# Performance work log

Measured on AMD Instinct MI355X. Metric: run time of the kernel, lower is better.

Reference implementation:

```python
import jax, jax.numpy as jnp
import numpy as np

B, S, H, NH = 2, 2048, 1024, 16
HD = H // NH  # 64
EPS = 1e-5


def setup_inputs() -> dict:
    key = jax.random.key(0)
    ks = jax.random.split(key, 4)
    return {
        "hidden_states": jax.random.normal(ks[0], (B, S, H), dtype=jnp.float32),
        "W_attn": jax.random.normal(ks[1], (H, 3 * H), dtype=jnp.float32) * (1.0 / np.sqrt(H)),
        "b_attn": jnp.zeros((3 * H,), dtype=jnp.float32),
        "W_proj": jax.random.normal(ks[2], (H, H), dtype=jnp.float32) * (1.0 / np.sqrt(H)),
        "b_proj": jnp.zeros((H,), dtype=jnp.float32),
        "q_gamma": jnp.ones((HD,), dtype=jnp.float32),
        "q_beta": jnp.zeros((HD,), dtype=jnp.float32),
        "k_gamma": jnp.ones((HD,), dtype=jnp.float32),
        "k_beta": jnp.zeros((HD,), dtype=jnp.float32),
    }


def _layernorm(x, gamma, beta):
    mu = jnp.mean(x, axis=-1, keepdims=True)
    var = jnp.mean(jnp.square(x - mu), axis=-1, keepdims=True)
    return (x - mu) * jax.lax.rsqrt(var + EPS) * gamma + beta


def reference(hidden_states, W_attn, b_attn, W_proj, b_proj, q_gamma, q_beta, k_gamma, k_beta):
    b, s, h = hidden_states.shape
    qkv = hidden_states @ W_attn + b_attn  # [B,S,3H]
    q, k, v = jnp.split(qkv, 3, axis=-1)
    # [B,S,H] -> [B,NH,S,HD]
    def to_heads(t):
        return t.reshape(b, s, NH, HD).transpose(0, 2, 1, 3)
    q, k, v = to_heads(q), to_heads(k), to_heads(v)
    # QK LayerNorm over head_dim
    q = _layernorm(q, q_gamma, q_beta)
    k = _layernorm(k, k_gamma, k_beta)
    scale = HD ** (-0.5)
    scores = jnp.einsum("bhqd,bhkd->bhqk", q, k) * scale
    causal = jnp.tril(jnp.ones((s, s), dtype=bool))
    mask_value = jnp.finfo(scores.dtype).min
    scores = jnp.where(causal, scores, mask_value)
    attn = jax.nn.softmax(scores.astype(jnp.float32), axis=-1).astype(q.dtype)
    out = jnp.einsum("bhqk,bhkd->bhqd", attn, v)
    out = out.transpose(0, 2, 1, 3).reshape(b, s, h)
    out = out @ W_proj + b_proj
    return out
```

## Files before the change

kernel.cpp:

```cpp
#include <hip/hip_runtime.h>
#include <hip/hip_bf16.h>

typedef __bf16 bf16x8 __attribute__((ext_vector_type(8)));
typedef float f32x4 __attribute__((ext_vector_type(4)));

#define EPS 1e-5f
#define QSCALE 0.18033688011112042f

__device__ __forceinline__ unsigned short f2bf(float f) {
  union { float f; unsigned int i; } c; c.f = f;
  unsigned int r = c.i + 0x7FFFu + ((c.i >> 16) & 1u);
  return (unsigned short)(r >> 16);
}
__device__ __forceinline__ unsigned short f2bf_t(float f) {
  union { float f; unsigned int i; } c; c.f = f;
  return (unsigned short)(c.i >> 16);
}

__device__ __forceinline__ void glds16(const void* g, void* l) {
  __builtin_amdgcn_global_load_lds(
      (const __attribute__((address_space(1))) unsigned int*)g,
      (__attribute__((address_space(3))) unsigned int*)l, 16, 0, 0);
}

__device__ __forceinline__ void transpose_tile(
    const float* __restrict__ in, unsigned short* __restrict__ out,
    int R, int C, int ct0, int rt0, unsigned short* S )
{
  const int t = threadIdx.x;
  const int r = t >> 2, c4 = (t & 3) * 16;
  {
    long base = (long)(rt0 + r) * C + ct0 + c4;
    float4 a = *(const float4*)&in[base];
    float4 b = *(const float4*)&in[base + 4];
    float4 c = *(const float4*)&in[base + 8];
    float4 d = *(const float4*)&in[base + 12];
    unsigned short v[16] = {f2bf(a.x), f2bf(a.y), f2bf(a.z), f2bf(a.w),
                            f2bf(b.x), f2bf(b.y), f2bf(b.z), f2bf(b.w),
                            f2bf(c.x), f2bf(c.y), f2bf(c.z), f2bf(c.w),
                            f2bf(d.x), f2bf(d.y), f2bf(d.z), f2bf(d.w)};
    *(uint4*)&S[r * 72 + c4]     = *(uint4*)&v[0];
    *(uint4*)&S[r * 72 + c4 + 8] = *(uint4*)&v[8];
  }
  __syncthreads();
  unsigned short tmp[16];
#pragma unroll
  for (int j = 0; j < 16; j++) tmp[j] = S[(c4 + j) * 72 + r];
  *(uint4*)&out[(long)(ct0 + r) * R + rt0 + c4]     = *(uint4*)&tmp[0];
  *(uint4*)&out[(long)(ct0 + r) * R + rt0 + c4 + 8] = *(uint4*)&tmp[8];
}

__global__ __launch_bounds__(256) void prep_kernel(
    const float* __restrict__ Wa, const float* __restrict__ Wp,
    const float* __restrict__ X,
    unsigned short* __restrict__ WaT, unsigned short* __restrict__ WpT,
    unsigned short* __restrict__ Xbf)
{
  __shared__ __align__(16) unsigned short S[64 * 72];
  const int id = blockIdx.x;
  if (id < 768) {
    transpose_tile(Wa, WaT, 1024, 3072, (id % 48) * 64, (id / 48) * 64, S);
  } else if (id < 1024) {
    const int i2 = id - 768;
    transpose_tile(Wp, WpT, 1024, 1024, (i2 % 16) * 64, (i2 / 16) * 64, S);
  } else {
    long i = ((long)(id - 1024) * 256 + threadIdx.x) * 16;
    float4 a = *(const float4*)&X[i];
    float4 b = *(const float4*)&X[i + 4];
    float4 c = *(const float4*)&X[i + 8];
    float4 d = *(const float4*)&X[i + 12];
    unsigned short v[16] = {f2bf(a.x), f2bf(a.y), f2bf(a.z), f2bf(a.w),
                            f2bf(b.x), f2bf(b.y), f2bf(b.z), f2bf(b.w),
                            f2bf(c.x), f2bf(c.y), f2bf(c.z), f2bf(c.w),
                            f2bf(d.x), f2bf(d.y), f2bf(d.z), f2bf(d.w)};
    *(uint4*)&Xbf[i]     = *(uint4*)&v[0];
    *(uint4*)&Xbf[i + 8] = *(uint4*)&v[8];
  }
}

__global__ __launch_bounds__(256) void qkvt_kernel(
    const float* __restrict__ Xf,
    const unsigned short* __restrict__ Xbf, int use_xbf,
    const unsigned short* __restrict__ WT,
    const float* __restrict__ bias,
    const float* __restrict__ qg, const float* __restrict__ qb,
    const float* __restrict__ kg, const float* __restrict__ kb,
    unsigned short* __restrict__ Qws, unsigned short* __restrict__ Kws,
    unsigned short* __restrict__ Vt)
{
  __shared__ __align__(16) unsigned short As[3][128 * 32];
  __shared__ __align__(16) unsigned short Bs[3][128 * 32];

  const int tid = threadIdx.x;
  const int w = tid >> 6, lane = tid & 63, quad = lane >> 4, l15 = lane & 15;
  const int mh = w & 1, nh = w >> 1;
  const int id = blockIdx.x;
  const int grow = lane >> 2, gcol = (lane & 3) * 8;

  f32x4 acc[4][4];
#pragma unroll
  for (int i = 0; i < 4; i++)
#pragma unroll
    for (int j = 0; j < 4; j++) acc[i][j] = (f32x4){0.f, 0.f, 0.f, 0.f};

  if (id < 512) {
    const int n0 = (id & 15) * 128, m0 = (id >> 4) * 128;

    if (use_xbf) {
      const long ga = (long)(m0 + w * 32 + grow) * 1024 + gcol;
      const long gb = (long)(n0 + w * 32 + grow) * 1024 + gcol;
#define STAGE_QK(bf, kk) do { \
        glds16(&Xbf[ga + (kk)],             &As[bf][(w * 32) * 32]); \
        glds16(&Xbf[ga + (kk) + 16 * 1024], &As[bf][(w * 32 + 16) * 32]); \
        glds16(&WT[gb + (kk)],              &Bs[bf][(w * 32) * 32]); \
        glds16(&WT[gb + (kk) + 16 * 1024],  &Bs[bf][(w * 32 + 16) * 32]); \
      } while (0)
      STAGE_QK(0, 0);
      STAGE_QK(1, 32);
      asm volatile("s_waitcnt vmcnt(4)" ::: "memory");
      __builtin_amdgcn_s_barrier();
      __builtin_amdgcn_sched_barrier(0);

      int cur = 0;
      for (int kt = 0; kt < 1024; kt += 32) {
        int stg = cur + 2; if (stg >= 3) stg -= 3;
        if (kt + 64 < 1024) STAGE_QK(stg, kt + 64);
        bf16x8 af[4], bfr[4];
#pragma unroll
        for (int mq = 0; mq < 4; mq++)
          af[mq] = *(const bf16x8*)&As[cur][(mh * 64 + mq * 16 + l15) * 32 + quad * 8];
#pragma unroll
        for (int nq = 0; nq < 4; nq++)
          bfr[nq] = *(const bf16x8*)&Bs[cur][(nh * 64 + nq * 16 + l15) * 32 + quad * 8];
#pragma unroll
        for (int mq = 0; mq < 4; mq++)
#pragma unroll
          for (int nq = 0; nq < 4; nq++)
            acc[mq][nq] = __builtin_amdgcn_mfma_f32_16x16x32_bf16(af[mq], bfr[nq], acc[mq][nq], 0, 0, 0);
        if (kt + 32 < 1024) {
          if (kt + 64 < 1024) asm volatile("s_waitcnt vmcnt(4)" ::: "memory");
          else                asm volatile("s_waitcnt vmcnt(0)" ::: "memory");
          __builtin_amdgcn_s_barrier();
          __builtin_amdgcn_sched_barrier(0);
        }
        cur = cur + 1; if (cur >= 3) cur -= 3;
      }
#undef STAGE_QK
    } else {
      const int sr2 = tid >> 1, sh2 = (tid & 1) * 16;
      {
        long xo = (long)(m0 + sr2) * 1024 + sh2;
        float4 a0 = *(const float4*)&Xf[xo];
        float4 a1 = *(const float4*)&Xf[xo + 4];
        float4 a2 = *(const float4*)&Xf[xo + 8];
        float4 a3 = *(const float4*)&Xf[xo + 12];
        unsigned short v[16] = {f2bf(a0.x), f2bf(a0.y), f2bf(a0.z), f2bf(a0.w),
                                f2bf(a1.x), f2bf(a1.y), f2bf(a1.z), f2bf(a1.w),
                                f2bf(a2.x), f2bf(a2.y), f2bf(a2.z), f2bf(a2.w),
                                f2bf(a3.x), f2bf(a3.y), f2bf(a3.z), f2bf(a3.w)};
        *(uint4*)&As[0][sr2 * 32 + sh2]     = *(uint4*)&v[0];
        *(uint4*)&As[0][sr2 * 32 + sh2 + 8] = *(uint4*)&v[8];
        long wo = (long)(n0 + sr2) * 1024 + sh2;
        *(uint4*)&Bs[0][sr2 * 32 + sh2]     = *(const uint4*)&WT[wo];
        *(uint4*)&Bs[0][sr2 * 32 + sh2 + 8] = *(const uint4*)&WT[wo + 8];
      }
      __syncthreads();

      int buf = 0;
      for (int kt = 0; kt < 1024; kt += 32) {
        const int nbuf = buf ^ 1;
        const bool pf = (kt + 32) < 1024;
        uint4 wv0, wv1;
        float4 a0, a1, a2, a3;
        if (pf) {
          long xo = (long)(m0 + sr2) * 1024 + kt + 32 + sh2;
          a0 = *(const float4*)&Xf[xo];
          a1 = *(const float4*)&Xf[xo + 4];
          a2 = *(const float4*)&Xf[xo + 8];
          a3 = *(const float4*)&Xf[xo + 12];
          long wo = (long)(n0 + sr2) * 1024 + kt + 32 + sh2;
          wv0 = *(const uint4*)&WT[wo];
          wv1 = *(const uint4*)&WT[wo + 8];
        }

        bf16x8 af[4], bfr[4];
#pragma unroll
        for (int mq = 0; mq < 4; mq++)
          af[mq] = *(const bf16x8*)&As[buf][(mh * 64 + mq * 16 + l15) * 32 + quad * 8];
#pragma unroll
        for (int nq = 0; nq < 4; nq++)
          bfr[nq] = *(const bf16x8*)&Bs[buf][(nh * 64 + nq * 16 + l15) * 32 + quad * 8];
#pragma unroll
        for (int mq = 0; mq < 4; mq++)
#pragma unroll
          for (int nq = 0; nq < 4; nq++)
            acc[mq][nq] = __builtin_amdgcn_mfma_f32_16x16x32_bf16(af[mq], bfr[nq], acc[mq][nq], 0, 0, 0);

        if (pf) {
          unsigned short v[16] = {f2bf(a0.x), f2bf(a0.y), f2bf(a0.z), f2bf(a0.w),
                                  f2bf(a1.x), f2bf(a1.y), f2bf(a1.z), f2bf(a1.w),
                                  f2bf(a2.x), f2bf(a2.y), f2bf(a2.z), f2bf(a2.w),
                                  f2bf(a3.x), f2bf(a3.y), f2bf(a3.z), f2bf(a3.w)};
          *(uint4*)&As[nbuf][sr2 * 32 + sh2]     = *(uint4*)&v[0];
          *(uint4*)&As[nbuf][sr2 * 32 + sh2 + 8] = *(uint4*)&v[8];
          *(uint4*)&Bs[nbuf][sr2 * 32 + sh2]     = wv0;
          *(uint4*)&Bs[nbuf][sr2 * 32 + sh2 + 8] = wv1;
        }
        __syncthreads();
        buf = nbuf;
      }
    }

#pragma unroll
    for (int nq = 0; nq < 4; nq++) {
      float bv = bias[n0 + nh * 64 + nq * 16 + l15];
#pragma unroll
      for (int mq = 0; mq < 4; mq++)
#pragma unroll
        for (int rr = 0; rr < 4; rr++) acc[mq][nq][rr] += bv;
    }

    const int g = (n0 >> 6) + nh;
    const bool isQ = g < 16;
    {
      float gv[4], bev[4];
#pragma unroll
      for (int nq = 0; nq < 4; nq++) {
        int d = nq * 16 + l15;
        gv[nq]  = isQ ? qg[d] : kg[d];
        bev[nq] = isQ ? qb[d] : kb[d];
        if (isQ) { gv[nq] *= QSCALE; bev[nq] *= QSCALE; }
      }
#pragma unroll
      for (int mq = 0; mq < 4; mq++)
#pragma unroll
        for (int rr = 0; rr < 4; rr++) {
          float s  = acc[mq][0][rr] + acc[mq][1][rr] + acc[mq][2][rr] + acc[mq][3][rr];
          float s2 = acc[mq][0][rr]*acc[mq][0][rr] + acc[mq][1][rr]*acc[mq][1][rr]
                   + acc[mq][2][rr]*acc[mq][2][rr] + acc[mq][3][rr]*acc[mq][3][rr];
#pragma unroll
          for (int off = 1; off < 16; off <<= 1) {
            s  += __shfl_xor(s,  off, 64);
            s2 += __shfl_xor(s2, off, 64);
          }
          float mu   = s * (1.0f / 64.0f);
          float var  = fmaxf(s2 * (1.0f / 64.0f) - mu * mu, 0.f);
          float rstd = rsqrtf(var + EPS);
#pragma unroll
          for (int nq = 0; nq < 4; nq++)
            acc[mq][nq][rr] = (acc[mq][nq][rr] - mu) * rstd * gv[nq] + bev[nq];
        }
    }

    unsigned short* dst = isQ ? Qws : Kws;
    const int head = isQ ? g : g - 16;
#pragma unroll
    for (int mq = 0; mq < 4; mq++)
#pragma unroll
      for (int rr = 0; rr < 4; rr++) {
        int m = m0 + mh * 64 + mq * 16 + quad * 4 + rr;
        int b = m >> 11, s = m & 2047;
        long base = ((long)((b * 16 + head) * 2048 + s)) * 64;
#pragma unroll
        for (int nq = 0; nq < 4; nq++)
          dst[base + nq * 16 + l15] = f2bf(acc[mq][nq][rr]);
      }
  } else {
    const int id2 = id - 512;
    const int n0 = (id2 & 15) * 128, m0 = ((id2 >> 4) & 7) * 128, bz = id2 >> 7;
    const long xrow0 = (long)bz * 2048;
    const unsigned short* WvT = WT + 2048L * 1024;

    if (use_xbf) {
      const long gva = (long)(m0 + w * 32 + grow) * 1024 + gcol;
      const long gvb = (xrow0 + n0 + w * 32 + grow) * 1024 + gcol;
#define STAGE_V(bf, kk) do { \
        glds16(&WvT[gva + (kk)],             &As[bf][(w * 32) * 32]); \
        glds16(&WvT[gva + (kk) + 16 * 1024], &As[bf][(w * 32 + 16) * 32]); \
        glds16(&Xbf[gvb + (kk)],             &Bs[bf][(w * 32) * 32]); \
        glds16(&Xbf[gvb + (kk) + 16 * 1024], &Bs[bf][(w * 32 + 16) * 32]); \
      } while (0)
      STAGE_V(0, 0);
      STAGE_V(1, 32);
      asm volatile("s_waitcnt vmcnt(4)" ::: "memory");
      __builtin_amdgcn_s_barrier();
      __builtin_amdgcn_sched_barrier(0);

      int cur = 0;
      for (int kt = 0; kt < 1024; kt += 32) {
        int stg = cur + 2; if (stg >= 3) stg -= 3;
        if (kt + 64 < 1024) STAGE_V(stg, kt + 64);
        bf16x8 af[4], bfr[4];
#pragma unroll
        for (int mq = 0; mq < 4; mq++)
          af[mq] = *(const bf16x8*)&As[cur][(mh * 64 + mq * 16 + l15) * 32 + quad * 8];
#pragma unroll
        for (int nq = 0; nq < 4; nq++)
          bfr[nq] = *(const bf16x8*)&Bs[cur][(nh * 64 + nq * 16 + l15) * 32 + quad * 8];
#pragma unroll
        for (int mq = 0; mq < 4; mq++)
#pragma unroll
          for (int nq = 0; nq < 4; nq++)
            acc[mq][nq] = __builtin_amdgcn_mfma_f32_16x16x32_bf16(af[mq], bfr[nq], acc[mq][nq], 0, 0, 0);
        if (kt + 32 < 1024) {
          if (kt + 64 < 1024) asm volatile("s_waitcnt vmcnt(4)" ::: "memory");
          else                asm volatile("s_waitcnt vmcnt(0)" ::: "memory");
          __builtin_amdgcn_s_barrier();
          __builtin_amdgcn_sched_barrier(0);
        }
        cur = cur + 1; if (cur >= 3) cur -= 3;
      }
#undef STAGE_V
    } else {
      const int sr2 = tid >> 1, sh2 = (tid & 1) * 16;
      {
        long wo = (long)(m0 + sr2) * 1024 + sh2;
        *(uint4*)&As[0][sr2 * 32 + sh2]     = *(const uint4*)&WvT[wo];
        *(uint4*)&As[0][sr2 * 32 + sh2 + 8] = *(const uint4*)&WvT[wo + 8];
        long xo = (xrow0 + n0 + sr2) * 1024 + sh2;
        float4 a0 = *(const float4*)&Xf[xo];
        float4 a1 = *(const float4*)&Xf[xo + 4];
        float4 a2 = *(const float4*)&Xf[xo + 8];
        float4 a3 = *(const float4*)&Xf[xo + 12];
        unsigned short v[16] = {f2bf(a0.x), f2bf(a0.y), f2bf(a0.z), f2bf(a0.w),
                                f2bf(a1.x), f2bf(a1.y), f2bf(a1.z), f2bf(a1.w),
                                f2bf(a2.x), f2bf(a2.y), f2bf(a2.z), f2bf(a2.w),
                                f2bf(a3.x), f2bf(a3.y), f2bf(a3.z), f2bf(a3.w)};
        *(uint4*)&Bs[0][sr2 * 32 + sh2]     = *(uint4*)&v[0];
        *(uint4*)&Bs[0][sr2 * 32 + sh2 + 8] = *(uint4*)&v[8];
      }
      __syncthreads();

      int buf = 0;
      for (int kt = 0; kt < 1024; kt += 32) {
        const int nbuf = buf ^ 1;
        const bool pf = (kt + 32) < 1024;
        uint4 wv0, wv1;
        float4 a0, a1, a2, a3;
        if (pf) {
          long wo = (long)(m0 + sr2) * 1024 + kt + 32 + sh2;
          wv0 = *(const uint4*)&WvT[wo];
          wv1 = *(const uint4*)&WvT[wo + 8];
          long xo = (xrow0 + n0 + sr2) * 1024 + kt + 32 + sh2;
          a0 = *(const float4*)&Xf[xo];
          a1 = *(const float4*)&Xf[xo + 4];
          a2 = *(const float4*)&Xf[xo + 8];
          a3 = *(const float4*)&Xf[xo + 12];
        }

        bf16x8 af[4], bfr[4];
#pragma unroll
        for (int mq = 0; mq < 4; mq++)
          af[mq] = *(const bf16x8*)&As[buf][(mh * 64 + mq * 16 + l15) * 32 + quad * 8];
#pragma unroll
        for (int nq = 0; nq < 4; nq++)
          bfr[nq] = *(const bf16x8*)&Bs[buf][(nh * 64 + nq * 16 + l15) * 32 + quad * 8];
#pragma unroll
        for (int mq = 0; mq < 4; mq++)
#pragma unroll
          for (int nq = 0; nq < 4; nq++)
            acc[mq][nq] = __builtin_amdgcn_mfma_f32_16x16x32_bf16(af[mq], bfr[nq], acc[mq][nq], 0, 0, 0);

        if (pf) {
          *(uint4*)&As[nbuf][sr2 * 32 + sh2]     = wv0;
          *(uint4*)&As[nbuf][sr2 * 32 + sh2 + 8] = wv1;
          unsigned short v[16] = {f2bf(a0.x), f2bf(a0.y), f2bf(a0.z), f2bf(a0.w),
                                  f2bf(a1.x), f2bf(a1.y), f2bf(a1.z), f2bf(a1.w),
                                  f2bf(a2.x), f2bf(a2.y), f2bf(a2.z), f2bf(a2.w),
                                  f2bf(a3.x), f2bf(a3.y), f2bf(a3.z), f2bf(a3.w)};
          *(uint4*)&Bs[nbuf][sr2 * 32 + sh2]     = *(uint4*)&v[0];
          *(uint4*)&Bs[nbuf][sr2 * 32 + sh2 + 8] = *(uint4*)&v[8];
        }
        __syncthreads();
        buf = nbuf;
      }
    }

    const long outb = (long)bz * 2097152;
#pragma unroll
    for (int mq = 0; mq < 4; mq++)
#pragma unroll
      for (int rr = 0; rr < 4; rr++) {
        int m = m0 + mh * 64 + mq * 16 + quad * 4 + rr;
        float bv = bias[2048 + m];
#pragma unroll
        for (int nq = 0; nq < 4; nq++) {
          int n = n0 + nh * 64 + nq * 16 + l15;
          Vt[outb + (long)m * 2048 + n] = f2bf(acc[mq][nq][rr] + bv);
        }
      }
  }
}

__global__ __launch_bounds__(256) void attn_kernel(
    unsigned short* __restrict__ Qws,
    const unsigned short* __restrict__ Kws,
    const unsigned short* __restrict__ Vt)
{
  __shared__ __align__(16) unsigned short Ks[2][64 * 72];
  __shared__ __align__(16) unsigned short VTs[2][64 * 72];
  __shared__ __align__(16) unsigned short Ps[64 * 64];

  const int tid = threadIdx.x;
  const int w = tid >> 6, lane = tid & 63, quad = lane >> 4, l15 = lane & 15;
  const int id = blockIdx.x;
  const int bh = (id & 7) * 4 + ((id >> 3) & 3);
  const int x  = id >> 5;
  const long bhoff = (long)bh * 2048 * 64;
  const long bhv   = (long)bh * 131072;

  const int sr = tid >> 2, sc = (tid & 3) * 16;
  const int qsw = ((sr >> 2) & 3) << 4;
  const int sw = ((l15 >> 2) & 3) << 4;
  const int pc0 = (quad * 8) ^ sw;
  const int pc1 = (32 + quad * 8) ^ sw;

  bf16x8 ones;
  {
    union { unsigned short u[8]; bf16x8 v; } c;
#pragma unroll
    for (int i = 0; i < 8; i++) c.u[i] = 0x3F80u;
    ones = c.v;
  }

#pragma unroll
  for (int ph = 0; ph < 2; ph++) {
    const int qt = ph ? (31 - x) : x;
    const int qbase = qt * 64;
    const int jmax = qt + 1;

    if (ph) __syncthreads();

    *(uint4*)&Ps[sr * 64 + (sc ^ qsw)]       = *(const uint4*)&Qws[bhoff + (qbase + sr) * 64 + sc];
    *(uint4*)&Ps[sr * 64 + ((sc ^ qsw) + 8)] = *(const uint4*)&Qws[bhoff + (qbase + sr) * 64 + sc + 8];
    *(uint4*)&Ks[0][sr * 72 + sc]      = *(const uint4*)&Kws[bhoff + sr * 64 + sc];
    *(uint4*)&Ks[0][sr * 72 + sc + 8]  = *(const uint4*)&Kws[bhoff + sr * 64 + sc + 8];
    *(uint4*)&VTs[0][sr * 72 + sc]     = *(const uint4*)&Vt[bhv + sr * 2048 + sc];
    *(uint4*)&VTs[0][sr * 72 + sc + 8] = *(const uint4*)&Vt[bhv + sr * 2048 + sc + 8];
    __syncthreads();

    const bf16x8 qf0 = *(const bf16x8*)&Ps[(w * 16 + l15) * 64 + pc0];
    const bf16x8 qf1 = *(const bf16x8*)&Ps[(w * 16 + l15) * 64 + pc1];

    f32x4 o[4], osum;
#pragma unroll
    for (int i = 0; i < 4; i++) o[i] = (f32x4){0.f, 0.f, 0.f, 0.f};
    osum = (f32x4){0.f, 0.f, 0.f, 0.f};

    int cb = 0;
    for (int j = 0; j < jmax; j++) {
      const int kb = j * 64;
      const bool pf = (j + 1) < jmax;
      uint4 pk0, pk1, pv0, pv1;
      if (pf) {
        const int kb1 = kb + 64;
        pk0 = *(const uint4*)&Kws[bhoff + (kb1 + sr) * 64 + sc];
        pk1 = *(const uint4*)&Kws[bhoff + (kb1 + sr) * 64 + sc + 8];
        pv0 = *(const uint4*)&Vt[bhv + sr * 2048 + kb1 + sc];
        pv1 = *(const uint4*)&Vt[bhv + sr * 2048 + kb1 + sc + 8];
      }

      f32x4 sacc[4];
#pragma unroll
      for (int i = 0; i < 4; i++) sacc[i] = (f32x4){0.f, 0.f, 0.f, 0.f};
#pragma unroll
      for (int nt = 0; nt < 4; nt++) {
        bf16x8 kf0 = *(const bf16x8*)&Ks[cb][(nt * 16 + l15) * 72 + quad * 8];
        bf16x8 kf1 = *(const bf16x8*)&Ks[cb][(nt * 16 + l15) * 72 + 32 + quad * 8];
        sacc[nt] = __builtin_amdgcn_mfma_f32_16x16x32_bf16(qf0, kf0, sacc[nt], 0, 0, 0);
        sacc[nt] = __builtin_amdgcn_mfma_f32_16x16x32_bf16(qf1, kf1, sacc[nt], 0, 0, 0);
      }

      const bool domask = (j == qt);
#pragma unroll
      for (int nt = 0; nt < 4; nt++)
#pragma unroll
        for (int rr = 0; rr < 4; rr++) {
          float p = exp2f(sacc[nt][rr]);
          if (domask) {
            int kcol = kb + nt * 16 + l15;
            int qrow = qbase + w * 16 + quad * 4 + rr;
            if (kcol > qrow) p = 0.f;
          }
          sacc[nt][rr] = p;
        }

#pragma unroll
      for (int rr = 0; rr < 4; rr++)
#pragma unroll
        for (int nt = 0; nt < 4; nt++)
          Ps[(w * 16 + quad * 4 + rr) * 64 + (((nt ^ quad) & 3) * 16 + l15)]
              = f2bf_t(sacc[nt][rr]);

      bf16x8 pfr0 = *(const bf16x8*)&Ps[(w * 16 + l15) * 64 + pc0];
      bf16x8 pfr1 = *(const bf16x8*)&Ps[(w * 16 + l15) * 64 + pc1];

      osum = __builtin_amdgcn_mfma_f32_16x16x32_bf16(pfr0, ones, osum, 0, 0, 0);
      osum = __builtin_amdgcn_mfma_f32_16x16x32_bf16(pfr1, ones, osum, 0, 0, 0);
#pragma unroll
      for (int dt = 0; dt < 4; dt++) {
        bf16x8 vf0 = *(const bf16x8*)&VTs[cb][(dt * 16 + l15) * 72 + quad * 8];
        bf16x8 vf1 = *(const bf16x8*)&VTs[cb][(dt * 16 + l15) * 72 + 32 + quad * 8];
        o[dt] = __builtin_amdgcn_mfma_f32_16x16x32_bf16(pfr0, vf0, o[dt], 0, 0, 0);
        o[dt] = __builtin_amdgcn_mfma_f32_16x16x32_bf16(pfr1, vf1, o[dt], 0, 0, 0);
      }

      if (pf) {
        const int nb = cb ^ 1;
        *(uint4*)&Ks[nb][sr * 72 + sc]      = pk0;
        *(uint4*)&Ks[nb][sr * 72 + sc + 8]  = pk1;
        *(uint4*)&VTs[nb][sr * 72 + sc]     = pv0;
        *(uint4*)&VTs[nb][sr * 72 + sc + 8] = pv1;
        __syncthreads();
        cb = nb;
      }
    }

#pragma unroll
    for (int rr = 0; rr < 4; rr++) {
      float inv = 1.0f / osum[rr];
      int row = qbase + w * 16 + quad * 4 + rr;
      long base = bhoff + (long)row * 64;
#pragma unroll
      for (int dt = 0; dt < 4; dt++)
        Qws[base + dt * 16 + l15] = f2bf(o[dt][rr] * inv);
    }
  }
}

__global__ __launch_bounds__(256) void proj_kernel(
    const unsigned short* __restrict__ AQ,
    const unsigned short* __restrict__ WT,
    const float* __restrict__ bias,
    float* __restrict__ Out)
{
  __shared__ __align__(16) unsigned short As[3][128 * 32];
  __shared__ __align__(16) unsigned short Bs[3][64 * 32];

  const int tid = threadIdx.x;
  const int w = tid >> 6, lane = tid & 63, quad = lane >> 4, l15 = lane & 15;
  const int mh = w & 1, nh = w >> 1;
  const int n0 = blockIdx.x * 64, m0 = blockIdx.y * 128;

  f32x4 acc[4][2];
#pragma unroll
  for (int i = 0; i < 4; i++)
#pragma unroll
    for (int j = 0; j < 2; j++) acc[i][j] = (f32x4){0.f, 0.f, 0.f, 0.f};

  const int grow = lane >> 2, gcolk = (lane & 3) * 8;
  const int m1 = m0 + w * 32 + grow, b1 = m1 >> 11, s1 = m1 & 2047;
  const int m2 = m1 + 16,            b2 = m2 >> 11, s2 = m2 & 2047;
  const long gpb = (long)(n0 + w * 16 + grow) * 1024 + gcolk;

#define STAGE_P(bf, kk) do { \
    int k_ = (kk) + gcolk, h_ = k_ >> 6, d_ = k_ & 63; \
    glds16(&AQ[((long)((b1 * 16 + h_) * 2048 + s1)) * 64 + d_], &As[bf][(w * 32) * 32]); \
    glds16(&AQ[((long)((b2 * 16 + h_) * 2048 + s2)) * 64 + d_], &As[bf][(w * 32 + 16) * 32]); \
    glds16(&WT[gpb + (kk)], &Bs[bf][(w * 16) * 32]); \
  } while (0)

  STAGE_P(0, 0);
  STAGE_P(1, 32);
  asm volatile("s_waitcnt vmcnt(3)" ::: "memory");
  __builtin_amdgcn_s_barrier();
  __builtin_amdgcn_sched_barrier(0);

  int cur = 0;
  for (int kt = 0; kt < 1024; kt += 32) {
    int stg = cur + 2; if (stg >= 3) stg -= 3;
    if (kt + 64 < 1024) STAGE_P(stg, kt + 64);
    bf16x8 af[4], bfr[2];
#pragma unroll
    for (int mq = 0; mq < 4; mq++)
      af[mq] = *(const bf16x8*)&As[cur][(mh * 64 + mq * 16 + l15) * 32 + quad * 8];
#pragma unroll
    for (int nq = 0; nq < 2; nq++)
      bfr[nq] = *(const bf16x8*)&Bs[cur][(nh * 32 + nq * 16 + l15) * 32 + quad * 8];
#pragma unroll
    for (int mq = 0; mq < 4; mq++)
#pragma unroll
      for (int nq = 0; nq < 2; nq++)
        acc[mq][nq] = __builtin_amdgcn_mfma_f32_16x16x32_bf16(af[mq], bfr[nq], acc[mq][nq], 0, 0, 0);
    if (kt + 32 < 1024) {
      if (kt + 64 < 1024) asm volatile("s_waitcnt vmcnt(3)" ::: "memory");
      else                asm volatile("s_waitcnt vmcnt(0)" ::: "memory");
      __builtin_amdgcn_s_barrier();
      __builtin_amdgcn_sched_barrier(0);
    }
    cur = cur + 1; if (cur >= 3) cur -= 3;
  }
#undef STAGE_P

#pragma unroll
  for (int nq = 0; nq < 2; nq++) {
    int n = n0 + nh * 32 + nq * 16 + l15;
    float bv = bias[n];
#pragma unroll
    for (int mq = 0; mq < 4; mq++)
#pragma unroll
      for (int rr = 0; rr < 4; rr++) {
        int mm = m0 + mh * 64 + mq * 16 + quad * 4 + rr;
        Out[(long)mm * 1024 + n] = acc[mq][nq][rr] + bv;
      }
  }
}

extern "C" void kernel_launch(void* const* d_in, const int* in_sizes, int n_in,
                              void* d_out, int out_size, void* d_ws, size_t ws_size,
                              hipStream_t stream) {
  const float* X  = (const float*)d_in[0];
  const float* Wa = (const float*)d_in[1];
  const float* ba = (const float*)d_in[2];
  const float* Wp = (const float*)d_in[3];
  const float* bp = (const float*)d_in[4];
  const float* qg = (const float*)d_in[5];
  const float* qb = (const float*)d_in[6];
  const float* kg = (const float*)d_in[7];
  const float* kb = (const float*)d_in[8];

  const long per = 2L * 16 * 2048 * 64;
  unsigned short* ws  = (unsigned short*)d_ws;
  unsigned short* Qws = ws;
  unsigned short* Kws = Qws + per;
  unsigned short* Vt  = Kws + per;

  const bool big = ws_size >= (size_t)(5L * per * 2);
  unsigned short *Xbf, *WaT, *WpT;
  if (big) {
    Xbf = Vt + per;
    WaT = Xbf + per;
    WpT = WaT + 3072L * 1024;
  } else {
    Xbf = Qws;
    WaT = Vt + per;
    WpT = WaT + 3072L * 1024;
  }

  prep_kernel<<<big ? 2048 : 1024, 256, 0, stream>>>(Wa, Wp, X, WaT, WpT, Xbf);
  qkvt_kernel<<<768, 256, 0, stream>>>(X, Xbf, big ? 1 : 0, WaT, ba,
                                       qg, qb, kg, kb, Qws, Kws, Vt);
  attn_kernel<<<512, 256, 0, stream>>>(Qws, Kws, Vt);
  proj_kernel<<<dim3(16, 32), 256, 0, stream>>>(Qws, WpT, bp, (float*)d_out);
}
```

Before: 212.7 us.

## Use double-buffered LDS in GEMMs and split attention into one query tile per block

The QKV and projection GEMMs drop from a three-stage global_load_lds pipeline with hand-placed vmcnt waits to a plain two-buffer scheme guarded by __syncthreads. This shrinks LDS use, which may allow more resident blocks, but each step now waits for all loads before computing, so less latency is hidden. Attention blocks no longer process two paired query tiles (x and 31-x) in sequence. The kernel launches 1024 blocks with one tile each, heaviest tiles first, trading the paired load balance for more parallelism.

```diff
diff --git a/kernel.cpp b/kernel.cpp
--- a/kernel.cpp
+++ b/kernel.cpp
@@ -88,8 +88,8 @@
     unsigned short* __restrict__ Qws, unsigned short* __restrict__ Kws,
     unsigned short* __restrict__ Vt)
 {
-  __shared__ __align__(16) unsigned short As[3][128 * 32];
-  __shared__ __align__(16) unsigned short Bs[3][128 * 32];
+  __shared__ __align__(16) unsigned short As[2][128 * 32];
+  __shared__ __align__(16) unsigned short Bs[2][128 * 32];
 
   const int tid = threadIdx.x;
   const int w = tid >> 6, lane = tid & 63, quad = lane >> 4, l15 = lane & 15;
@@ -116,34 +116,24 @@
         glds16(&WT[gb + (kk) + 16 * 1024],  &Bs[bf][(w * 32 + 16) * 32]); \
       } while (0)
       STAGE_QK(0, 0);
-      STAGE_QK(1, 32);
-      asm volatile("s_waitcnt vmcnt(4)" ::: "memory");
-      __builtin_amdgcn_s_barrier();
-      __builtin_amdgcn_sched_barrier(0);
-
-      int cur = 0;
+      __syncthreads();
+      int buf = 0;
       for (int kt = 0; kt < 1024; kt += 32) {
-        int stg = cur + 2; if (stg >= 3) stg -= 3;
-        if (kt + 64 < 1024) STAGE_QK(stg, kt + 64);
+        if (kt + 32 < 1024) STAGE_QK(buf ^ 1, kt + 32);
         bf16x8 af[4], bfr[4];
 #pragma unroll
         for (int mq = 0; mq < 4; mq++)
-          af[mq] = *(const bf16x8*)&As[cur][(mh * 64 + mq * 16 + l15) * 32 + quad * 8];
+          af[mq] = *(const bf16x8*)&As[buf][(mh * 64 + mq * 16 + l15) * 32 + quad * 8];
 #pragma unroll
         for (int nq = 0; nq < 4; nq++)
-          bfr[nq] = *(const bf16x8*)&Bs[cur][(nh * 64 + nq * 16 + l15) * 32 + quad * 8];
+          bfr[nq] = *(const bf16x8*)&Bs[buf][(nh * 64 + nq * 16 + l15) * 32 + quad * 8];
 #pragma unroll
         for (int mq = 0; mq < 4; mq++)
 #pragma unroll
           for (int nq = 0; nq < 4; nq++)
             acc[mq][nq] = __builtin_amdgcn_mfma_f32_16x16x32_bf16(af[mq], bfr[nq], acc[mq][nq], 0, 0, 0);
-        if (kt + 32 < 1024) {
-          if (kt + 64 < 1024) asm volatile("s_waitcnt vmcnt(4)" ::: "memory");
-          else                asm volatile("s_waitcnt vmcnt(0)" ::: "memory");
-          __builtin_amdgcn_s_barrier();
-          __builtin_amdgcn_sched_barrier(0);
-        }
-        cur = cur + 1; if (cur >= 3) cur -= 3;
+        __syncthreads();
+        buf ^= 1;
       }
 #undef STAGE_QK
     } else {
@@ -281,34 +271,24 @@
         glds16(&Xbf[gvb + (kk) + 16 * 1024], &Bs[bf][(w * 32 + 16) * 32]); \
       } while (0)
       STAGE_V(0, 0);
-      STAGE_V(1, 32);
-      asm volatile("s_waitcnt vmcnt(4)" ::: "memory");
-      __builtin_amdgcn_s_barrier();
-      __builtin_amdgcn_sched_barrier(0);
-
-      int cur = 0;
+      __syncthreads();
+      int buf = 0;
       for (int kt = 0; kt < 1024; kt += 32) {
-        int stg = cur + 2; if (stg >= 3) stg -= 3;
-        if (kt + 64 < 1024) STAGE_V(stg, kt + 64);
+        if (kt + 32 < 1024) STAGE_V(buf ^ 1, kt + 32);
         bf16x8 af[4], bfr[4];
 #pragma unroll
         for (int mq = 0; mq < 4; mq++)
-          af[mq] = *(const bf16x8*)&As[cur][(mh * 64 + mq * 16 + l15) * 32 + quad * 8];
+          af[mq] = *(const bf16x8*)&As[buf][(mh * 64 + mq * 16 + l15) * 32 + quad * 8];
 #pragma unroll
         for (int nq = 0; nq < 4; nq++)
-          bfr[nq] = *(const bf16x8*)&Bs[cur][(nh * 64 + nq * 16 + l15) * 32 + quad * 8];
+          bfr[nq] = *(const bf16x8*)&Bs[buf][(nh * 64 + nq * 16 + l15) * 32 + quad * 8];
 #pragma unroll
         for (int mq = 0; mq < 4; mq++)
 #pragma unroll
           for (int nq = 0; nq < 4; nq++)
             acc[mq][nq] = __builtin_amdgcn_mfma_f32_16x16x32_bf16(af[mq], bfr[nq], acc[mq][nq], 0, 0, 0);
-        if (kt + 32 < 1024) {
-          if (kt + 64 < 1024) asm volatile("s_waitcnt vmcnt(4)" ::: "memory");
-          else                asm volatile("s_waitcnt vmcnt(0)" ::: "memory");
-          __builtin_amdgcn_s_barrier();
-          __builtin_amdgcn_sched_barrier(0);
-        }
-        cur = cur + 1; if (cur >= 3) cur -= 3;
+        __syncthreads();
+        buf ^= 1;
       }
 #undef STAGE_V
     } else {
@@ -405,7 +385,7 @@
   const int w = tid >> 6, lane = tid & 63, quad = lane >> 4, l15 = lane & 15;
   const int id = blockIdx.x;
   const int bh = (id & 7) * 4 + ((id >> 3) & 3);
-  const int x  = id >> 5;
+  const int qt = 31 - (id >> 5);
   const long bhoff = (long)bh * 2048 * 64;
   const long bhv   = (long)bh * 131072;
 
@@ -423,108 +403,102 @@
     ones = c.v;
   }
 
-#pragma unroll
-  for (int ph = 0; ph < 2; ph++) {
-    const int qt = ph ? (31 - x) : x;
-    const int qbase = qt * 64;
-    const int jmax = qt + 1;
-
-    if (ph) __syncthreads();
-
-    *(uint4*)&Ps[sr * 64 + (sc ^ qsw)]       = *(const uint4*)&Qws[bhoff + (qbase + sr) * 64 + sc];
-    *(uint4*)&Ps[sr * 64 + ((sc ^ qsw) + 8)] = *(const uint4*)&Qws[bhoff + (qbase + sr) * 64 + sc + 8];
-    *(uint4*)&Ks[0][sr * 72 + sc]      = *(const uint4*)&Kws[bhoff + sr * 64 + sc];
-    *(uint4*)&Ks[0][sr * 72 + sc + 8]  = *(const uint4*)&Kws[bhoff + sr * 64 + sc + 8];
-    *(uint4*)&VTs[0][sr * 72 + sc]     = *(const uint4*)&Vt[bhv + sr * 2048 + sc];
-    *(uint4*)&VTs[0][sr * 72 + sc + 8] = *(const uint4*)&Vt[bhv + sr * 2048 + sc + 8];
-    __syncthreads();
-
-    const bf16x8 qf0 = *(const bf16x8*)&Ps[(w * 16 + l15) * 64 + pc0];
-    const bf16x8 qf1 = *(const bf16x8*)&Ps[(w * 16 + l15) * 64 + pc1];
-
-    f32x4 o[4], osum;
-#pragma unroll
-    for (int i = 0; i < 4; i++) o[i] = (f32x4){0.f, 0.f, 0.f, 0.f};
-    osum = (f32x4){0.f, 0.f, 0.f, 0.f};
-
-    int cb = 0;
-    for (int j = 0; j < jmax; j++) {
-      const int kb = j * 64;
-      const bool pf = (j + 1) < jmax;
-      uint4 pk0, pk1, pv0, pv1;
-      if (pf) {
-        const int kb1 = kb + 64;
-        pk0 = *(const uint4*)&Kws[bhoff + (kb1 + sr) * 64 + sc];
-        pk1 = *(const uint4*)&Kws[bhoff + (kb1 + sr) * 64 + sc + 8];
-        pv0 = *(const uint4*)&Vt[bhv + sr * 2048 + kb1 + sc];
-        pv1 = *(const uint4*)&Vt[bhv + sr * 2048 + kb1 + sc + 8];
-      }
-
-      f32x4 sacc[4];
-#pragma unroll
-      for (int i = 0; i < 4; i++) sacc[i] = (f32x4){0.f, 0.f, 0.f, 0.f};
-#pragma unroll
-      for (int nt = 0; nt < 4; nt++) {
-        bf16x8 kf0 = *(const bf16x8*)&Ks[cb][(nt * 16 + l15) * 72 + quad * 8];
-        bf16x8 kf1 = *(const bf16x8*)&Ks[cb][(nt * 16 + l15) * 72 + 32 + quad * 8];
-        sacc[nt] = __builtin_amdgcn_mfma_f32_16x16x32_bf16(qf0, kf0, sacc[nt], 0, 0, 0);
-        sacc[nt] = __builtin_amdgcn_mfma_f32_16x16x32_bf16(qf1, kf1, sacc[nt], 0, 0, 0);
-      }
-
-      const bool domask = (j == qt);
+  const int qbase = qt * 64;
+  const int jmax = qt + 1;
+
+  *(uint4*)&Ps[sr * 64 + (sc ^ qsw)]       = *(const uint4*)&Qws[bhoff + (qbase + sr) * 64 + sc];
+  *(uint4*)&Ps[sr * 64 + ((sc ^ qsw) + 8)] = *(const uint4*)&Qws[bhoff + (qbase + sr) * 64 + sc + 8];
+  *(uint4*)&Ks[0][sr * 72 + sc]      = *(const uint4*)&Kws[bhoff + sr * 64 + sc];
+  *(uint4*)&Ks[0][sr * 72 + sc + 8]  = *(const uint4*)&Kws[bhoff + sr * 64 + sc + 8];
+  *(uint4*)&VTs[0][sr * 72 + sc]     = *(const uint4*)&Vt[bhv + sr * 2048 + sc];
+  *(uint4*)&VTs[0][sr * 72 + sc + 8] = *(const uint4*)&Vt[bhv + sr * 2048 + sc + 8];
+  __syncthreads();
+
+  const bf16x8 qf0 = *(const bf16x8*)&Ps[(w * 16 + l15) * 64 + pc0];
+  const bf16x8 qf1 = *(const bf16x8*)&Ps[(w * 16 + l15) * 64 + pc1];
+
+  f32x4 o[4], osum;
+#pragma unroll
+  for (int i = 0; i < 4; i++) o[i] = (f32x4){0.f, 0.f, 0.f, 0.f};
+  osum = (f32x4){0.f, 0.f, 0.f, 0.f};
+
+  int cb = 0;
+  for (int j = 0; j < jmax; j++) {
+    const int kb = j * 64;
+    const bool pf = (j + 1) < jmax;
+    uint4 pk0, pk1, pv0, pv1;
+    if (pf) {
+      const int kb1 = kb + 64;
+      pk0 = *(const uint4*)&Kws[bhoff + (kb1 + sr) * 64 + sc];
+      pk1 = *(const uint4*)&Kws[bhoff + (kb1 + sr) * 64 + sc + 8];
+      pv0 = *(const uint4*)&Vt[bhv + sr * 2048 + kb1 + sc];
+      pv1 = *(const uint4*)&Vt[bhv + sr * 2048 + kb1 + sc + 8];
+    }
+
+    f32x4 sacc[4];
+#pragma unroll
+    for (int i = 0; i < 4; i++) sacc[i] = (f32x4){0.f, 0.f, 0.f, 0.f};
+#pragma unroll
+    for (int nt = 0; nt < 4; nt++) {
+      bf16x8 kf0 = *(const bf16x8*)&Ks[cb][(nt * 16 + l15) * 72 + quad * 8];
+      bf16x8 kf1 = *(const bf16x8*)&Ks[cb][(nt * 16 + l15) * 72 + 32 + quad * 8];
+      sacc[nt] = __builtin_amdgcn_mfma_f32_16x16x32_bf16(qf0, kf0, sacc[nt], 0, 0, 0);
+      sacc[nt] = __builtin_amdgcn_mfma_f32_16x16x32_bf16(qf1, kf1, sacc[nt], 0, 0, 0);
+    }
+
+    const bool domask = (j == qt);
+#pragma unroll
+    for (int nt = 0; nt < 4; nt++)
+#pragma unroll
+      for (int rr = 0; rr < 4; rr++) {
+        float p = exp2f(sacc[nt][rr]);
+        if (domask) {
+          int kcol = kb + nt * 16 + l15;
+          int qrow = qbase + w * 16 + quad * 4 + rr;
+          if (kcol > qrow) p = 0.f;
+        }
+        sacc[nt][rr] = p;
+      }
+
+#pragma unroll
+    for (int rr = 0; rr < 4; rr++)
 #pragma unroll
       for (int nt = 0; nt < 4; nt++)
-#pragma unroll
-        for (int rr = 0; rr < 4; rr++) {
-          float p = exp2f(sacc[nt][rr]);
-          if (domask) {
-            int kcol = kb + nt * 16 + l15;
-            int qrow = qbase + w * 16 + quad * 4 + rr;
-            if (kcol > qrow) p = 0.f;
-          }
-          sacc[nt][rr] = p;
-        }
-
-#pragma unroll
-      for (int rr = 0; rr < 4; rr++)
-#pragma unroll
-        for (int nt = 0; nt < 4; nt++)
-          Ps[(w * 16 + quad * 4 + rr) * 64 + (((nt ^ quad) & 3) * 16 + l15)]
-              = f2bf_t(sacc[nt][rr]);
-
-      bf16x8 pfr0 = *(const bf16x8*)&Ps[(w * 16 + l15) * 64 + pc0];
-      bf16x8 pfr1 = *(const bf16x8*)&Ps[(w * 16 + l15) * 64 + pc1];
-
-      osum = __builtin_amdgcn_mfma_f32_16x16x32_bf16(pfr0, ones, osum, 0, 0, 0);
-      osum = __builtin_amdgcn_mfma_f32_16x16x32_bf16(pfr1, ones, osum, 0, 0, 0);
-#pragma unroll
-      for (int dt = 0; dt < 4; dt++) {
-        bf16x8 vf0 = *(const bf16x8*)&VTs[cb][(dt * 16 + l15) * 72 + quad * 8];
-        bf16x8 vf1 = *(const bf16x8*)&VTs[cb][(dt * 16 + l15) * 72 + 32 + quad * 8];
-        o[dt] = __builtin_amdgcn_mfma_f32_16x16x32_bf16(pfr0, vf0, o[dt], 0, 0, 0);
-        o[dt] = __builtin_amdgcn_mfma_f32_16x16x32_bf16(pfr1, vf1, o[dt], 0, 0, 0);
-      }
-
-      if (pf) {
-        const int nb = cb ^ 1;
-        *(uint4*)&Ks[nb][sr * 72 + sc]      = pk0;
-        *(uint4*)&Ks[nb][sr * 72 + sc + 8]  = pk1;
-        *(uint4*)&VTs[nb][sr * 72 + sc]     = pv0;
-        *(uint4*)&VTs[nb][sr * 72 + sc + 8] = pv1;
-        __syncthreads();
-        cb = nb;
-      }
-    }
-
-#pragma unroll
-    for (int rr = 0; rr < 4; rr++) {
-      float inv = 1.0f / osum[rr];
-      int row = qbase + w * 16 + quad * 4 + rr;
-      long base = bhoff + (long)row * 64;
-#pragma unroll
-      for (int dt = 0; dt < 4; dt++)
-        Qws[base + dt * 16 + l15] = f2bf(o[dt][rr] * inv);
-    }
+        Ps[(w * 16 + quad * 4 + rr) * 64 + (((nt ^ quad) & 3) * 16 + l15)]
+            = f2bf_t(sacc[nt][rr]);
+
+    bf16x8 pfr0 = *(const bf16x8*)&Ps[(w * 16 + l15) * 64 + pc0];
+    bf16x8 pfr1 = *(const bf16x8*)&Ps[(w * 16 + l15) * 64 + pc1];
+
+    osum = __builtin_amdgcn_mfma_f32_16x16x32_bf16(pfr0, ones, osum, 0, 0, 0);
+    osum = __builtin_amdgcn_mfma_f32_16x16x32_bf16(pfr1, ones, osum, 0, 0, 0);
+#pragma unroll
+    for (int dt = 0; dt < 4; dt++) {
+      bf16x8 vf0 = *(const bf16x8*)&VTs[cb][(dt * 16 + l15) * 72 + quad * 8];
+      bf16x8 vf1 = *(const bf16x8*)&VTs[cb][(dt * 16 + l15) * 72 + 32 + quad * 8];
+      o[dt] = __builtin_amdgcn_mfma_f32_16x16x32_bf16(pfr0, vf0, o[dt], 0, 0, 0);
+      o[dt] = __builtin_amdgcn_mfma_f32_16x16x32_bf16(pfr1, vf1, o[dt], 0, 0, 0);
+    }
+
+    if (pf) {
+      const int nb = cb ^ 1;
+      *(uint4*)&Ks[nb][sr * 72 + sc]      = pk0;
+      *(uint4*)&Ks[nb][sr * 72 + sc + 8]  = pk1;
+      *(uint4*)&VTs[nb][sr * 72 + sc]     = pv0;
+      *(uint4*)&VTs[nb][sr * 72 + sc + 8] = pv1;
+      __syncthreads();
+      cb = nb;
+    }
+  }
+
+#pragma unroll
+  for (int rr = 0; rr < 4; rr++) {
+    float inv = 1.0f / osum[rr];
+    int row = qbase + w * 16 + quad * 4 + rr;
+    long base = bhoff + (long)row * 64;
+#pragma unroll
+    for (int dt = 0; dt < 4; dt++)
+      Qws[base + dt * 16 + l15] = f2bf(o[dt][rr] * inv);
   }
 }
 
@@ -534,8 +508,8 @@
     const float* __restrict__ bias,
     float* __restrict__ Out)
 {
-  __shared__ __align__(16) unsigned short As[3][128 * 32];
-  __shared__ __align__(16) unsigned short Bs[3][64 * 32];
+  __shared__ __align__(16) unsigned short As[2][128 * 32];
+  __shared__ __align__(16) unsigned short Bs[2][64 * 32];
 
   const int tid = threadIdx.x;
   const int w = tid >> 6, lane = tid & 63, quad = lane >> 4, l15 = lane & 15;
@@ -561,34 +535,24 @@
   } while (0)
 
   STAGE_P(0, 0);
-  STAGE_P(1, 32);
-  asm volatile("s_waitcnt vmcnt(3)" ::: "memory");
-  __builtin_amdgcn_s_barrier();
-  __builtin_amdgcn_sched_barrier(0);
-
-  int cur = 0;
+  __syncthreads();
+  int buf = 0;
   for (int kt = 0; kt < 1024; kt += 32) {
-    int stg = cur + 2; if (stg >= 3) stg -= 3;
-    if (kt + 64 < 1024) STAGE_P(stg, kt + 64);
+    if (kt + 32 < 1024) STAGE_P(buf ^ 1, kt + 32);
     bf16x8 af[4], bfr[2];
 #pragma unroll
     for (int mq = 0; mq < 4; mq++)
-      af[mq] = *(const bf16x8*)&As[cur][(mh * 64 + mq * 16 + l15) * 32 + quad * 8];
+      af[mq] = *(const bf16x8*)&As[buf][(mh * 64 + mq * 16 + l15) * 32 + quad * 8];
 #pragma unroll
     for (int nq = 0; nq < 2; nq++)
-      bfr[nq] = *(const bf16x8*)&Bs[cur][(nh * 32 + nq * 16 + l15) * 32 + quad * 8];
+      bfr[nq] = *(const bf16x8*)&Bs[buf][(nh * 32 + nq * 16 + l15) * 32 + quad * 8];
 #pragma unroll
     for (int mq = 0; mq < 4; mq++)
 #pragma unroll
       for (int nq = 0; nq < 2; nq++)
         acc[mq][nq] = __builtin_amdgcn_mfma_f32_16x16x32_bf16(af[mq], bfr[nq], acc[mq][nq], 0, 0, 0);
-    if (kt + 32 < 1024) {
-      if (kt + 64 < 1024) asm volatile("s_waitcnt vmcnt(3)" ::: "memory");
-      else                asm volatile("s_waitcnt vmcnt(0)" ::: "memory");
-      __builtin_amdgcn_s_barrier();
-      __builtin_amdgcn_sched_barrier(0);
-    }
-    cur = cur + 1; if (cur >= 3) cur -= 3;
+    __syncthreads();
+    buf ^= 1;
   }
 #undef STAGE_P
 
@@ -640,6 +604,6 @@
   prep_kernel<<<big ? 2048 : 1024, 256, 0, stream>>>(Wa, Wp, X, WaT, WpT, Xbf);
   qkvt_kernel<<<768, 256, 0, stream>>>(X, Xbf, big ? 1 : 0, WaT, ba,
                                        qg, qb, kg, kb, Qws, Kws, Vt);
-  attn_kernel<<<512, 256, 0, stream>>>(Qws, Kws, Vt);
+  attn_kernel<<<1024, 256, 0, stream>>>(Qws, Kws, Vt);
   proj_kernel<<<dim3(16, 32), 256, 0, stream>>>(Qws, WpT, bp, (float*)d_out);
 }
```

New measurement: 212.8 us. About the same (+0.0%).
